# Optimization experiments

Measured on AMD Instinct MI355X. Metric: run time of the kernel, lower is better.

## Reference

```python
import jax, jax.numpy as jnp
import numpy as np

D = 256   # koopman_dim
B = 256   # batch of initial latent states
T_STEPS = 512
DT = 0.01


def setup_inputs() -> dict:
    key = jax.random.key(0)
    k1, k2 = jax.random.split(key)
    z0 = jax.random.normal(k1, (B, D), dtype=jnp.float32)
    # nnx.Linear default lecun_normal init: std ~ 1/sqrt(fan_in)
    kernel = jax.random.normal(k2, (D, D), dtype=jnp.float32) / jnp.sqrt(jnp.float32(D))
    log_dt = jnp.asarray(jnp.log(DT), dtype=jnp.float32)
    return {"z0": z0, "kernel": kernel, "log_dt": log_dt, "T": T_STEPS}


def reference(z0, kernel, log_dt, T):
    dt = jnp.exp(log_dt)
    eye = jnp.eye(kernel.shape[0], dtype=kernel.dtype)
    # Bilinear / Tustin discretization: K_d = (I - 0.5*dt*K)^-1 (I + 0.5*dt*K)
    K_discrete = jnp.linalg.solve(eye - 0.5 * dt * kernel, eye + 0.5 * dt * kernel)

    def step(z, _):
        z_next = z @ K_discrete  # [B, D] @ [D, D]
        return z_next, z_next

    _, preds = jax.lax.scan(step, z0, None, length=T)  # preds: [T, B, D]
    return jnp.transpose(preds, (1, 0, 2))  # [B, T, D]
```

## Files before the change

### kernel.cpp

```cpp
#include <hip/hip_runtime.h>


#define DD 256
#define TT 512
#define MATF (DD * DD)
#define LDT ((size_t)TT * (size_t)DD)

typedef __attribute__((ext_vector_type(8))) short bf16x8;
typedef __attribute__((ext_vector_type(4))) float f32x4;

#define GLD16(g, l)                                                  \
    __builtin_amdgcn_global_load_lds(                                \
        (const __attribute__((address_space(1))) void*)(g),          \
        (__attribute__((address_space(3))) void*)(l), 16, 0, 0)

static __device__ __forceinline__ unsigned short f2bf(float f) {
    unsigned int u = __float_as_uint(f);
    u += 0x7fffu + ((u >> 16) & 1u);
    return (unsigned short)(u >> 16);
}
static __device__ __forceinline__ unsigned pack2bf(float a, float b) {
    return (unsigned)f2bf(a) | ((unsigned)f2bf(b) << 16);
}

__device__ __forceinline__ void g32_core(const float* __restrict__ Ab, int lda,
                                         const float* __restrict__ Bb, int ldb,
                                         int rowBase, int colBase, float acc[2][2]) {
    __shared__ __align__(16) float As[64 * 38];
    __shared__ __align__(16) float Bs[64 * 40];
    const int tid = threadIdx.x;
    const int tx = tid & 15, ty = tid >> 4;
    const int am = tid >> 4;
    const int ak = (tid & 15) << 2;
    const int bk = tid >> 3;
    const int bn = (tid & 7) << 2;

    acc[0][0] = acc[0][1] = acc[1][0] = acc[1][1] = 0.f;

    float4 pa0 = *(const float4*)(Ab + (size_t)(rowBase + am) * lda + ak);
    float4 pa1 = *(const float4*)(Ab + (size_t)(rowBase + am + 16) * lda + ak);
    float4 pb0 = *(const float4*)(Bb + (size_t)bk * ldb + colBase + bn);
    float4 pb1 = *(const float4*)(Bb + (size_t)(bk + 32) * ldb + colBase + bn);

    for (int k0 = 0; k0 < DD; k0 += 64) {
        As[(ak + 0) * 38 + am] = pa0.x;
        As[(ak + 1) * 38 + am] = pa0.y;
        As[(ak + 2) * 38 + am] = pa0.z;
        As[(ak + 3) * 38 + am] = pa0.w;
        As[(ak + 0) * 38 + am + 16] = pa1.x;
        As[(ak + 1) * 38 + am + 16] = pa1.y;
        As[(ak + 2) * 38 + am + 16] = pa1.z;
        As[(ak + 3) * 38 + am + 16] = pa1.w;
        *(float4*)(&Bs[bk * 40 + bn]) = pb0;
        *(float4*)(&Bs[(bk + 32) * 40 + bn]) = pb1;
        __syncthreads();
        if (k0 + 64 < DD) {
            pa0 = *(const float4*)(Ab + (size_t)(rowBase + am) * lda + k0 + 64 + ak);
            pa1 = *(const float4*)(Ab + (size_t)(rowBase + am + 16) * lda + k0 + 64 + ak);
            pb0 = *(const float4*)(Bb + (size_t)(bk + k0 + 64) * ldb + colBase + bn);
            pb1 = *(const float4*)(Bb + (size_t)(bk + 32 + k0 + 64) * ldb + colBase + bn);
        }
#pragma unroll
        for (int kk = 0; kk < 64; ++kk) {
            float2 a2 = *(const float2*)(&As[kk * 38 + (ty << 1)]);
            float2 b2 = *(const float2*)(&Bs[kk * 40 + (tx << 1)]);
            acc[0][0] = fmaf(a2.x, b2.x, acc[0][0]);
            acc[0][1] = fmaf(a2.x, b2.y, acc[0][1]);
            acc[1][0] = fmaf(a2.y, b2.x, acc[1][0]);
            acc[1][1] = fmaf(a2.y, b2.y, acc[1][1]);
        }
        __syncthreads();
    }
}

__global__ void __launch_bounds__(256)
n1_kernel(const float* __restrict__ K, const float* __restrict__ log_dt,
          const float* __restrict__ z0, float* __restrict__ A2,
          float* __restrict__ Bop, unsigned short* __restrict__ Zb0) {
    const float cs = 0.5f * expf(log_dt[0]);
    {
        int b = ((blockIdx.y * 8 + blockIdx.x) * 256 + threadIdx.x) * 4;
        uint2 w;
        w.x = pack2bf(z0[b], z0[b + 1]);
        w.y = pack2bf(z0[b + 2], z0[b + 3]);
        *(uint2*)(Zb0 + b) = w;
    }
    float acc[2][2];
    const int rowBase = blockIdx.y << 5, colBase = blockIdx.x << 5;
    g32_core(K, DD, K, DD, rowBase, colBase, acc);
    const float cs2 = cs * cs;
    const int r0 = rowBase + ((threadIdx.x >> 4) << 1);
    const int c0 = colBase + ((threadIdx.x & 15) << 1);
#pragma unroll
    for (int i = 0; i < 2; ++i) {
        int r = r0 + i;
        float e0 = K[(size_t)r * DD + c0], e1 = K[(size_t)r * DD + c0 + 1];
        float p0 = cs2 * acc[i][0], p1 = cs2 * acc[i][1];
        *(float2*)(A2 + (size_t)r * DD + c0) = (float2){p0, p1};
        float2 w;
        w.x = 2.f * p0 + 2.f * cs * e0 + (r == c0 ? 2.f : 0.f);
        w.y = 2.f * p1 + 2.f * cs * e1 + (r == c0 + 1 ? 2.f : 0.f);
        *(float2*)(Bop + (size_t)r * DD + c0) = w;
    }
}

__global__ void __launch_bounds__(256)
n2_kernel(const float* __restrict__ A2, const float* __restrict__ Bop,
          const float* __restrict__ K, const float* __restrict__ log_dt,
          float* __restrict__ E) {
    const float cs = 0.5f * expf(log_dt[0]);
    float acc[2][2];
    const int rowBase = blockIdx.y << 5, colBase = blockIdx.x << 5;
    g32_core(A2, DD, Bop, DD, rowBase, colBase, acc);
    const int r0 = rowBase + ((threadIdx.x >> 4) << 1);
    const int c0 = colBase + ((threadIdx.x & 15) << 1);
#pragma unroll
    for (int i = 0; i < 2; ++i) {
        int r = r0 + i;
        float e0 = K[(size_t)r * DD + c0], e1 = K[(size_t)r * DD + c0 + 1];
        float2 v;
        v.x = acc[i][0] + 2.f * cs * e0;
        v.y = acc[i][1] + 2.f * cs * e1;
        *(float2*)(E + (size_t)r * DD + c0) = v;
    }
}

__global__ void __launch_bounds__(256)
gpow_kernel(const float* __restrict__ A, const float* __restrict__ B,
            float* __restrict__ C, long long sA, long long sB, long long sC) {
    float acc[2][2];
    const int rowBase = blockIdx.y << 5, colBase = blockIdx.x << 5;
    g32_core(A + blockIdx.z * sA, DD, B + blockIdx.z * sB, DD, rowBase, colBase, acc);
    float* Cb = C + blockIdx.z * sC;
    const int r0 = rowBase + ((threadIdx.x >> 4) << 1);
    const int c0 = colBase + ((threadIdx.x & 15) << 1);
#pragma unroll
    for (int i = 0; i < 2; ++i) {
        int r = r0 + i;
        *(float2*)(Cb + (size_t)r * DD + c0) = (float2){acc[i][0], acc[i][1]};
    }
}

__global__ void __launch_bounds__(256)
gpow4_kernel(float* __restrict__ Epow) {
    static const int sa[4] = {1, 2, 2, 3};
    static const int sb[4] = {2, 2, 3, 3};
    static const int sc[4] = {4, 5, 6, 7};
    const int z = blockIdx.z;
    float acc[2][2];
    const int rowBase = blockIdx.y << 5, colBase = blockIdx.x << 5;
    g32_core(Epow + (size_t)sa[z] * MATF, DD, Epow + (size_t)sb[z] * MATF, DD,
             rowBase, colBase, acc);
    float* Cb = Epow + (size_t)sc[z] * MATF;
    const int r0 = rowBase + ((threadIdx.x >> 4) << 1);
    const int c0 = colBase + ((threadIdx.x & 15) << 1);
#pragma unroll
    for (int i = 0; i < 2; ++i) {
        int r = r0 + i;
        *(float2*)(Cb + (size_t)r * DD + c0) = (float2){acc[i][0], acc[i][1]};
    }
}

__global__ void __launch_bounds__(256)
comb_kernel(const float* __restrict__ Epow, unsigned short* __restrict__ MTb,
            float* __restrict__ W1, float* __restrict__ W2,
            float* __restrict__ W3) {
    __shared__ float tle[8][32][33];
    const int tid = threadIdx.x;
    const int k0 = blockIdx.y << 5, c0 = blockIdx.x << 5;
    const int ltx = tid & 31, lty = tid >> 5;
#pragma unroll
    for (int m = 0; m < 8; ++m)
#pragma unroll
        for (int it = 0; it < 4; ++it) {
            int k = lty + (it << 3);
            tle[m][ltx][k] =
                Epow[(size_t)m * MATF + (size_t)(k0 + k) * DD + c0 + ltx];
        }
    __syncthreads();

    const int c = tid >> 3;
    const int kb = (tid & 7) << 2;
    float em[8][4];
#pragma unroll
    for (int m = 0; m < 8; ++m)
#pragma unroll
        for (int u = 0; u < 4; ++u) em[m][u] = tle[m][c][kb + u];

    float diag[4];
#pragma unroll
    for (int u = 0; u < 4; ++u)
        diag[u] = ((k0 + kb + u) == (c0 + c)) ? 1.f : 0.f;

    float w32[4];
    for (int j = 1; j <= 32; ++j) {
        float val[4] = {diag[0], diag[1], diag[2], diag[3]};
        long long coef = 1;
#pragma unroll
        for (int m = 1; m <= 8; ++m) {
            coef = coef * (j - m + 1) / m;
            float cf = (float)(coef < 0 ? 0 : coef);
#pragma unroll
            for (int u = 0; u < 4; ++u) val[u] = fmaf(cf, em[m - 1][u], val[u]);
        }
        uint2 w;
        w.x = pack2bf(val[0], val[1]);
        w.y = pack2bf(val[2], val[3]);
        *(uint2*)(MTb + (size_t)(j - 1) * MATF + (size_t)(c0 + c) * DD + k0 + kb) = w;
        if (j == 32) {
            w32[0] = val[0]; w32[1] = val[1]; w32[2] = val[2]; w32[3] = val[3];
        }
    }
    float w64[4] = {diag[0], diag[1], diag[2], diag[3]};
    float w96[4] = {diag[0], diag[1], diag[2], diag[3]};
    {
        double c64 = 1.0, c96 = 1.0;
#pragma unroll
        for (int m = 1; m <= 8; ++m) {
            c64 = c64 * (double)(64 - m + 1) / (double)m;
            c96 = c96 * (double)(96 - m + 1) / (double)m;
            float f64 = (float)c64, f96 = (float)c96;
#pragma unroll
            for (int u = 0; u < 4; ++u) {
                w64[u] = fmaf(f64, em[m - 1][u], w64[u]);
                w96[u] = fmaf(f96, em[m - 1][u], w96[u]);
            }
        }
    }
    float* tw = &tle[0][0][0];
    const int wk = tid >> 3, wc = (tid & 7) << 2;
    float* Wd[3] = {W1, W2, W3};
    float* Ws[3] = {w32, w64, w96};
#pragma unroll
    for (int p = 0; p < 3; ++p) {
        __syncthreads();
#pragma unroll
        for (int u = 0; u < 4; ++u) tw[(kb + u) * 33 + c] = Ws[p][u];
        __syncthreads();
        float4 v = {tw[wk * 33 + wc], tw[wk * 33 + wc + 1],
                    tw[wk * 33 + wc + 2], tw[wk * 33 + wc + 3]};
        *(float4*)(Wd[p] + (size_t)(k0 + wk) * DD + c0 + wc) = v;
    }
}

__global__ void __launch_bounds__(256)
scan3_kernel(const float* __restrict__ z0, float* __restrict__ Zf,
             const float* __restrict__ W1, const float* __restrict__ W2,
             const float* __restrict__ W3, float* __restrict__ Wtab,
             unsigned short* __restrict__ Zb, int level) {
    static const signed char JA[3][7] = {{0, 0, 0, 17, 18, 0, 0},
                                         {0, 1, 2, 3, 2, 3, 20},
                                         {4, 5, 0, 1, 2, 3, 0}};
    static const signed char JB[3][7] = {{0, 1, 2, 1, 2, 0, 0},
                                         {3, 3, 3, 3, 4, 4, 4},
                                         {4, 4, 5, 5, 5, 5, 0}};
    static const signed char JD[3][7] = {{1, 2, 3, 19, 20, 0, 0},
                                         {4, 5, 6, 7, 8, 9, 21},
                                         {10, 11, 12, 13, 14, 15, 0}};
    const float* Wp[6] = {W1, W2, W3, Wtab, Wtab + MATF, Wtab + 2 * (size_t)MATF};
    const int jz = blockIdx.z;
    const int a = JA[level][jz], b = JB[level][jz], d = JD[level][jz];

    const float* Asrc;
    if (a == 0) Asrc = z0;
    else if (a < 16) Asrc = Zf + (size_t)a * MATF;
    else Asrc = Wp[a - 16];

    float acc[2][2];
    const int rowBase = blockIdx.y << 5, colBase = blockIdx.x << 5;
    g32_core(Asrc, DD, Wp[b], DD, rowBase, colBase, acc);

    const int r0 = rowBase + ((threadIdx.x >> 4) << 1);
    const int c0 = colBase + ((threadIdx.x & 15) << 1);
    if (d < 16) {
        float* Zo32 = Zf + (size_t)d * MATF;
        unsigned short* Zo = Zb + (size_t)d * MATF;
#pragma unroll
        for (int ii = 0; ii < 2; ++ii) {
            int r = r0 + ii;
            float2 v = {acc[ii][0], acc[ii][1]};
            *(float2*)(Zo32 + (size_t)r * DD + c0) = v;
            *(unsigned*)(Zo + (size_t)r * DD + c0) = pack2bf(v.x, v.y);
        }
    } else {
        float* Cb = Wtab + (size_t)(d - 19) * MATF;
#pragma unroll
        for (int ii = 0; ii < 2; ++ii) {
            int r = r0 + ii;
            *(float2*)(Cb + (size_t)r * DD + c0) = (float2){acc[ii][0], acc[ii][1]};
        }
    }
}

__global__ void __launch_bounds__(256)
fill_kernel(const unsigned short* __restrict__ Zb,
            const unsigned short* __restrict__ MTb,
            float* __restrict__ out) {
    __shared__ __align__(16) char pool[32768];
    const int zz = blockIdx.z;
    const int i = zz & 15;
    const int j = (zz >> 4) + 1;
    const int t = i * 32 + j - 1;
    const unsigned short* Zt = Zb + (size_t)i * MATF;
    const unsigned short* MT = MTb + (size_t)(j - 1) * MATF;

    const int tid = threadIdx.x;
    const int lane = tid & 63, wid = tid >> 6;
    const int rowBase = blockIdx.y * 128, colBase = blockIdx.x * 128;
    const int wr = (wid >> 1) * 64, wc = (wid & 1) * 64;

    int rowq[4], skq[4], ldsb[4];
#pragma unroll
    for (int q = 0; q < 4; ++q) {
        int c = q * 256 + wid * 64 + lane;
        int row = c >> 3;
        rowq[q] = row;
        skq[q] = ((c ^ (row & 7)) & 7) << 3;
        ldsb[q] = (q * 256 + wid * 64) << 4;
    }

    f32x4 acc[4][4];
#pragma unroll
    for (int a = 0; a < 4; ++a)
#pragma unroll
        for (int b = 0; b < 4; ++b) acc[a][b] = (f32x4){0.f, 0.f, 0.f, 0.f};

    auto stage = [&](int k0) {
#pragma unroll
        for (int q = 0; q < 4; ++q) {
            GLD16(Zt + (size_t)(rowBase + rowq[q]) * DD + k0 + skq[q], pool + ldsb[q]);
            GLD16(MT + (size_t)(colBase + rowq[q]) * DD + k0 + skq[q],
                  pool + 16384 + ldsb[q]);
        }
    };

    stage(0);
    for (int r = 0; r < 4; ++r) {
        __syncthreads();
        const char* asb = pool;
        const char* bsb = pool + 16384;
#pragma unroll
        for (int ks = 0; ks < 2; ++ks) {
            bf16x8 af[4], bg[4];
            const int kk = ks * 32 + (lane >> 4) * 8;
#pragma unroll
            for (int f = 0; f < 4; ++f) {
                int rr = wr + f * 16 + (lane & 15);
                af[f] = *(const bf16x8*)(asb + ((rr * 128 + kk * 2) ^ ((rr & 7) << 4)));
                int cc = wc + f * 16 + (lane & 15);
                bg[f] = *(const bf16x8*)(bsb + ((cc * 128 + kk * 2) ^ ((cc & 7) << 4)));
            }
#pragma unroll
            for (int fr = 0; fr < 4; ++fr)
#pragma unroll
                for (int fc = 0; fc < 4; ++fc)
                    acc[fr][fc] = __builtin_amdgcn_mfma_f32_16x16x32_bf16(
                        af[fr], bg[fc], acc[fr][fc], 0, 0, 0);
        }
        __syncthreads();
        if (r < 3) stage((r + 1) * 64);
    }

    float* Cs = (float*)pool;
    float* C = out + (size_t)t * DD;
#pragma unroll
    for (int hp = 0; hp < 2; ++hp) {
        __syncthreads();
        if (wr == hp * 64) {
#pragma unroll
            for (int fr = 0; fr < 4; ++fr) {
#pragma unroll
                for (int fc = 0; fc < 4; ++fc) {
                    int ccol = wc + fc * 16 + (lane & 15);
#pragma unroll
                    for (int ii = 0; ii < 4; ++ii) {
                        int lr = fr * 16 + ((lane >> 4) << 2) + ii;
                        int csw = ccol ^ (((lr >> 2) & 1) << 4);
                        Cs[lr * 128 + csw] = acc[fr][fc][ii];
                    }
                }
            }
        }
        __syncthreads();
#pragma unroll
        for (int it = 0; it < 8; ++it) {
            int chunk = it * 256 + tid;
            int row = chunk >> 5;
            int c4 = (chunk & 31) << 2;
            int csw = c4 ^ (((row >> 2) & 1) << 4);
            float4 v = *(const float4*)(Cs + row * 128 + csw);
            *(float4*)(C + (size_t)(rowBase + hp * 64 + row) * LDT + colBase + c4) = v;
        }
    }
}

__global__ void prep_kernel(const float* __restrict__ K,
                            const float* __restrict__ log_dt,
                            float* __restrict__ A) {
    int idx = blockIdx.x * blockDim.x + threadIdx.x;
    A[idx] = 0.5f * expf(log_dt[0]) * K[idx];
}

template <int EPI>
__global__ void __launch_bounds__(256)
g32_kernel(const float* A, const float* B, float* C, const float* E, float* C2,
           int lda, int ldb, int ldc, long long sA, long long sB, long long sC) {
    float acc[2][2];
    const int rowBase = blockIdx.y << 5, colBase = blockIdx.x << 5;
    g32_core(A + blockIdx.z * sA, lda, B + blockIdx.z * sB, ldb, rowBase, colBase, acc);
    float* Cb = C + blockIdx.z * sC;
    const int r0 = rowBase + ((threadIdx.x >> 4) << 1);
    const int c0 = colBase + ((threadIdx.x & 15) << 1);
#pragma unroll
    for (int i = 0; i < 2; ++i) {
        int r = r0 + i;
        float2 v;
        if (EPI == 2) {
            float e0 = E[(size_t)r * DD + c0], e1 = E[(size_t)r * DD + c0 + 1];
            v.x = acc[i][0] + 2.f * e0 + (r == c0 ? 1.f : 0.f);
            v.y = acc[i][1] + 2.f * e1 + (r == c0 + 1 ? 1.f : 0.f);
        } else {
            v.x = acc[i][0];
            v.y = acc[i][1];
        }
        *(float2*)(Cb + (size_t)r * ldc + c0) = v;
        if (EPI == 1) {
            float e0 = E[(size_t)r * DD + c0], e1 = E[(size_t)r * DD + c0 + 1];
            float2 w;
            w.x = 2.f * acc[i][0] + 2.f * e0 + (r == c0 ? 2.f : 0.f);
            w.y = 2.f * acc[i][1] + 2.f * e1 + (r == c0 + 1 ? 2.f : 0.f);
            *(float2*)(C2 + (size_t)r * DD + c0) = w;
        }
    }
}

extern "C" void kernel_launch(void* const* d_in, const int* in_sizes, int n_in,
                              void* d_out, int out_size, void* d_ws, size_t ws_size,
                              hipStream_t stream) {
    const float* z0 = (const float*)d_in[0];
    const float* Kmat = (const float*)d_in[1];
    const float* log_dt = (const float*)d_in[2];
    float* out = (float*)d_out;

    dim3 blk(256);

    float* A2 = (float*)d_ws;
    float* Bop = A2 + MATF;
    float* Epow = Bop + MATF;
    float* W1 = Epow + (size_t)8 * MATF;
    float* W2 = W1 + MATF;
    float* W3 = W2 + MATF;
    float* Wtab = W3 + MATF;
    float* Zf = Wtab + (size_t)3 * MATF;
    unsigned short* MTb = (unsigned short*)(Zf + (size_t)16 * MATF);
    unsigned short* Zb = MTb + (size_t)32 * MATF;
    const size_t need = (size_t)32 * MATF * 4 + (size_t)48 * MATF * 2;

    if (ws_size >= need) {
        dim3 g(8, 8, 1);
        n1_kernel<<<g, blk, 0, stream>>>(Kmat, log_dt, z0, A2, Bop, Zb);
        n2_kernel<<<g, blk, 0, stream>>>(A2, Bop, Kmat, log_dt, Epow);

        gpow_kernel<<<g, blk, 0, stream>>>(Epow, Epow, Epow + MATF, 0, 0, 0);
        gpow_kernel<<<dim3(8, 8, 2), blk, 0, stream>>>(
            Epow, Epow + MATF, Epow + 2 * (size_t)MATF, MATF, 0, MATF);
        gpow4_kernel<<<dim3(8, 8, 4), blk, 0, stream>>>(Epow);

        comb_kernel<<<g, blk, 0, stream>>>(Epow, MTb, W1, W2, W3);

        const int njobs[3] = {5, 7, 6};
        for (int s = 0; s < 3; ++s)
            scan3_kernel<<<dim3(8, 8, njobs[s]), blk, 0, stream>>>(
                z0, Zf, W1, W2, W3, Wtab, Zb, s);

        fill_kernel<<<dim3(2, 2, 512), blk, 0, stream>>>(Zb, MTb, out);
        return;
    }

    float* A = (float*)d_ws;
    float* A2f = A + MATF;
    float* Bopf = A2f + MATF;
    float* Kd = Bopf + MATF;
    prep_kernel<<<MATF / 256, blk, 0, stream>>>(Kmat, log_dt, A);
    dim3 g(8, 8, 1);
    g32_kernel<1><<<g, blk, 0, stream>>>(A, A, A2f, A, Bopf, DD, DD, DD, 0, 0, 0);
    g32_kernel<2><<<g, blk, 0, stream>>>(A2f, Bopf, Kd, A, (float*)0, DD, DD, DD, 0, 0, 0);
    for (int t = 0; t < TT; ++t) {
        const float* Ain = (t == 0) ? z0 : out + (size_t)(t - 1) * DD;
        int lda = (t == 0) ? DD : (int)LDT;
        g32_kernel<0><<<g, blk, 0, stream>>>(Ain, Kd, out + (size_t)t * DD,
                                             (const float*)0, (float*)0,
                                             lda, DD, (int)LDT, 0, 0, 0);
    }
}
```

Baseline: 115.0 us.

## Build K_d powers from raw K powers with precomputed series coefficients

Rather than forming E = K_d - I through two GEMM kernels (n1, n2) and then taking its powers, the code now takes powers of the raw kernel K directly, K^1..K^8. Each K_d^j - I is then expanded as a degree-8 polynomial in K, with coefficients (binomial times negative-binomial series, scaled by (dt/2)^m) computed in double precision into a shared table inside comb_kernel. This removes one dependent 256x256 GEMM launch from the serial setup chain and folds the z0 bf16 conversion into comb_kernel. It relies on the truncated series in K matching the earlier truncation accuracy.

Result: faster. 103.3 us (-10.2%).

```diff
diff --git a/kernel.cpp b/kernel.cpp
--- a/kernel.cpp
+++ b/kernel.cpp
@@ -74,54 +74,21 @@
 }
 
 __global__ void __launch_bounds__(256)
-n1_kernel(const float* __restrict__ K, const float* __restrict__ log_dt,
-          const float* __restrict__ z0, float* __restrict__ A2,
-          float* __restrict__ Bop, unsigned short* __restrict__ Zb0) {
-    const float cs = 0.5f * expf(log_dt[0]);
+p1_kernel(const float* __restrict__ K, float* __restrict__ Pw) {
     {
         int b = ((blockIdx.y * 8 + blockIdx.x) * 256 + threadIdx.x) * 4;
-        uint2 w;
-        w.x = pack2bf(z0[b], z0[b + 1]);
-        w.y = pack2bf(z0[b + 2], z0[b + 3]);
-        *(uint2*)(Zb0 + b) = w;
+        *(float4*)(Pw + b) = *(const float4*)(K + b);
     }
     float acc[2][2];
     const int rowBase = blockIdx.y << 5, colBase = blockIdx.x << 5;
     g32_core(K, DD, K, DD, rowBase, colBase, acc);
-    const float cs2 = cs * cs;
+    float* Cb = Pw + MATF;
     const int r0 = rowBase + ((threadIdx.x >> 4) << 1);
     const int c0 = colBase + ((threadIdx.x & 15) << 1);
 #pragma unroll
     for (int i = 0; i < 2; ++i) {
         int r = r0 + i;
-        float e0 = K[(size_t)r * DD + c0], e1 = K[(size_t)r * DD + c0 + 1];
-        float p0 = cs2 * acc[i][0], p1 = cs2 * acc[i][1];
-        *(float2*)(A2 + (size_t)r * DD + c0) = (float2){p0, p1};
-        float2 w;
-        w.x = 2.f * p0 + 2.f * cs * e0 + (r == c0 ? 2.f : 0.f);
-        w.y = 2.f * p1 + 2.f * cs * e1 + (r == c0 + 1 ? 2.f : 0.f);
-        *(float2*)(Bop + (size_t)r * DD + c0) = w;
-    }
-}
-
-__global__ void __launch_bounds__(256)
-n2_kernel(const float* __restrict__ A2, const float* __restrict__ Bop,
-          const float* __restrict__ K, const float* __restrict__ log_dt,
-          float* __restrict__ E) {
-    const float cs = 0.5f * expf(log_dt[0]);
-    float acc[2][2];
-    const int rowBase = blockIdx.y << 5, colBase = blockIdx.x << 5;
-    g32_core(A2, DD, Bop, DD, rowBase, colBase, acc);
-    const int r0 = rowBase + ((threadIdx.x >> 4) << 1);
-    const int c0 = colBase + ((threadIdx.x & 15) << 1);
-#pragma unroll
-    for (int i = 0; i < 2; ++i) {
-        int r = r0 + i;
-        float e0 = K[(size_t)r * DD + c0], e1 = K[(size_t)r * DD + c0 + 1];
-        float2 v;
-        v.x = acc[i][0] + 2.f * cs * e0;
-        v.y = acc[i][1] + 2.f * cs * e1;
-        *(float2*)(E + (size_t)r * DD + c0) = v;
+        *(float2*)(Cb + (size_t)r * DD + c0) = (float2){acc[i][0], acc[i][1]};
     }
 }
 
@@ -142,16 +109,16 @@
 }
 
 __global__ void __launch_bounds__(256)
-gpow4_kernel(float* __restrict__ Epow) {
+gpow4_kernel(float* __restrict__ Pw) {
     static const int sa[4] = {1, 2, 2, 3};
     static const int sb[4] = {2, 2, 3, 3};
     static const int sc[4] = {4, 5, 6, 7};
     const int z = blockIdx.z;
     float acc[2][2];
     const int rowBase = blockIdx.y << 5, colBase = blockIdx.x << 5;
-    g32_core(Epow + (size_t)sa[z] * MATF, DD, Epow + (size_t)sb[z] * MATF, DD,
+    g32_core(Pw + (size_t)sa[z] * MATF, DD, Pw + (size_t)sb[z] * MATF, DD,
              rowBase, colBase, acc);
-    float* Cb = Epow + (size_t)sc[z] * MATF;
+    float* Cb = Pw + (size_t)sc[z] * MATF;
     const int r0 = rowBase + ((threadIdx.x >> 4) << 1);
     const int c0 = colBase + ((threadIdx.x & 15) << 1);
 #pragma unroll
@@ -162,12 +129,46 @@
 }
 
 __global__ void __launch_bounds__(256)
-comb_kernel(const float* __restrict__ Epow, unsigned short* __restrict__ MTb,
+comb_kernel(const float* __restrict__ Pw, const float* __restrict__ log_dt,
+            const float* __restrict__ z0, unsigned short* __restrict__ MTb,
             float* __restrict__ W1, float* __restrict__ W2,
-            float* __restrict__ W3) {
+            float* __restrict__ W3, unsigned short* __restrict__ Zb0) {
     __shared__ float tle[8][32][33];
+    __shared__ float gtab[34][8];
     const int tid = threadIdx.x;
     const int k0 = blockIdx.y << 5, c0 = blockIdx.x << 5;
+    const float csf = 0.5f * expf(log_dt[0]);
+
+    {
+        int b = ((blockIdx.y * 8 + blockIdx.x) * 256 + tid) * 4;
+        uint2 w;
+        w.x = pack2bf(z0[b], z0[b + 1]);
+        w.y = pack2bf(z0[b + 2], z0[b + 3]);
+        *(uint2*)(Zb0 + b) = w;
+    }
+
+    if (tid < 34) {
+        int j = (tid < 32) ? (tid + 1) : ((tid == 32) ? 64 : 96);
+        double b[9], cq[9];
+        b[0] = 1.0;
+        cq[0] = 1.0;
+#pragma unroll
+        for (int p = 1; p <= 8; ++p) {
+            b[p] = b[p - 1] * (double)(j - p + 1) / (double)p;
+            cq[p] = cq[p - 1] * (double)(j + p - 1) / (double)p;
+        }
+        double csm = (double)csf;
+#pragma unroll
+        for (int m = 1; m <= 8; ++m) {
+            double s = 0.0;
+#pragma unroll
+            for (int p = 0; p <= 8; ++p)
+                if (p <= m) s += b[p] * cq[m - p];
+            gtab[tid][m - 1] = (float)(s * csm);
+            csm *= (double)csf;
+        }
+    }
+
     const int ltx = tid & 31, lty = tid >> 5;
 #pragma unroll
     for (int m = 0; m < 8; ++m)
@@ -175,7 +176,7 @@
         for (int it = 0; it < 4; ++it) {
             int k = lty + (it << 3);
             tle[m][ltx][k] =
-                Epow[(size_t)m * MATF + (size_t)(k0 + k) * DD + c0 + ltx];
+                Pw[(size_t)m * MATF + (size_t)(k0 + k) * DD + c0 + ltx];
         }
     __syncthreads();
 
@@ -195,14 +196,11 @@
     float w32[4];
     for (int j = 1; j <= 32; ++j) {
         float val[4] = {diag[0], diag[1], diag[2], diag[3]};
-        long long coef = 1;
-#pragma unroll
-        for (int m = 1; m <= 8; ++m) {
-            coef = coef * (j - m + 1) / m;
-            float cf = (float)(coef < 0 ? 0 : coef);
-#pragma unroll
-            for (int u = 0; u < 4; ++u) val[u] = fmaf(cf, em[m - 1][u], val[u]);
-        }
+        const float* gj = gtab[j - 1];
+#pragma unroll
+        for (int m = 0; m < 8; ++m)
+#pragma unroll
+            for (int u = 0; u < 4; ++u) val[u] = fmaf(gj[m], em[m][u], val[u]);
         uint2 w;
         w.x = pack2bf(val[0], val[1]);
         w.y = pack2bf(val[2], val[3]);
@@ -213,20 +211,14 @@
     }
     float w64[4] = {diag[0], diag[1], diag[2], diag[3]};
     float w96[4] = {diag[0], diag[1], diag[2], diag[3]};
-    {
-        double c64 = 1.0, c96 = 1.0;
-#pragma unroll
-        for (int m = 1; m <= 8; ++m) {
-            c64 = c64 * (double)(64 - m + 1) / (double)m;
-            c96 = c96 * (double)(96 - m + 1) / (double)m;
-            float f64 = (float)c64, f96 = (float)c96;
-#pragma unroll
-            for (int u = 0; u < 4; ++u) {
-                w64[u] = fmaf(f64, em[m - 1][u], w64[u]);
-                w96[u] = fmaf(f96, em[m - 1][u], w96[u]);
-            }
-        }
-    }
+#pragma unroll
+    for (int m = 0; m < 8; ++m)
+#pragma unroll
+        for (int u = 0; u < 4; ++u) {
+            w64[u] = fmaf(gtab[32][m], em[m][u], w64[u]);
+            w96[u] = fmaf(gtab[33][m], em[m][u], w96[u]);
+        }
+
     float* tw = &tle[0][0][0];
     const int wk = tid >> 3, wc = (tid & 7) << 2;
     float* Wd[3] = {W1, W2, W3};
@@ -444,29 +436,24 @@
 
     dim3 blk(256);
 
-    float* A2 = (float*)d_ws;
-    float* Bop = A2 + MATF;
-    float* Epow = Bop + MATF;
-    float* W1 = Epow + (size_t)8 * MATF;
+    float* Pw = (float*)d_ws;
+    float* W1 = Pw + (size_t)8 * MATF;
     float* W2 = W1 + MATF;
     float* W3 = W2 + MATF;
     float* Wtab = W3 + MATF;
     float* Zf = Wtab + (size_t)3 * MATF;
     unsigned short* MTb = (unsigned short*)(Zf + (size_t)16 * MATF);
     unsigned short* Zb = MTb + (size_t)32 * MATF;
-    const size_t need = (size_t)32 * MATF * 4 + (size_t)48 * MATF * 2;
+    const size_t need = (size_t)30 * MATF * 4 + (size_t)48 * MATF * 2;
 
     if (ws_size >= need) {
         dim3 g(8, 8, 1);
-        n1_kernel<<<g, blk, 0, stream>>>(Kmat, log_dt, z0, A2, Bop, Zb);
-        n2_kernel<<<g, blk, 0, stream>>>(A2, Bop, Kmat, log_dt, Epow);
-
-        gpow_kernel<<<g, blk, 0, stream>>>(Epow, Epow, Epow + MATF, 0, 0, 0);
+        p1_kernel<<<g, blk, 0, stream>>>(Kmat, Pw);
         gpow_kernel<<<dim3(8, 8, 2), blk, 0, stream>>>(
-            Epow, Epow + MATF, Epow + 2 * (size_t)MATF, MATF, 0, MATF);
-        gpow4_kernel<<<dim3(8, 8, 4), blk, 0, stream>>>(Epow);
-
-        comb_kernel<<<g, blk, 0, stream>>>(Epow, MTb, W1, W2, W3);
+            Pw, Pw + MATF, Pw + 2 * (size_t)MATF, MATF, 0, MATF);
+        gpow4_kernel<<<dim3(8, 8, 4), blk, 0, stream>>>(Pw);
+
+        comb_kernel<<<g, blk, 0, stream>>>(Pw, log_dt, z0, MTb, W1, W2, W3, Zb);
 
         const int njobs[3] = {5, 7, 6};
         for (int s = 0; s < 3; ++s)
```
